# Optimization experiments

Hardware: AMD Instinct MI355X
Metric: run time of the kernel (lower is better)

The kernel has to match this reference:

```python
import jax, jax.numpy as jnp
import numpy as np

B, S, C = 4, 1024, 1024
HD = 64          # hard-coded head dim in the module
H = C // HD      # 16 heads
ROT = 32         # RotaryEmbedding hard-codes Dim=32 (partial rotary)
EPS = 1e-4       # pnormalize eps


def pnormalize(w, parts):
    # torch: reshape(parts, -1, *w.shape[1:]); vector_norm over trailing dims;
    # alpha = sqrt(n.numel()/partitioned.numel()) = 1/sqrt(fan_in); w / (eps + alpha*n)
    p = w.reshape(parts, -1, w.shape[-1])
    n = jnp.linalg.norm(p, axis=-1, keepdims=True)
    alpha = np.sqrt(n.size / p.size)
    return (p / (EPS + alpha * n)).reshape(w.shape)


def mp_linear(x, w, parts):
    fan_in = w.shape[-1]
    return x @ (pnormalize(w, parts) / np.sqrt(fan_in)).T


def rotate_half(t):
    t1, t2 = jnp.split(t, 2, axis=-1)
    return jnp.concatenate([-t2, t1], axis=-1)


def apply_rope(t, freqs):
    return t * jnp.cos(freqs) + rotate_half(t) * jnp.sin(freqs)


def setup_inputs() -> dict:
    key = jax.random.key(0)
    k1, k2, k3, k4 = jax.random.split(key, 4)
    x = jax.random.normal(k1, (B, S, C), jnp.float32)
    w_qkv = jax.random.normal(k2, (3 * C, C), jnp.float32)   # MPLinear init: std=1
    w_out = jax.random.normal(k3, (C, C), jnp.float32)
    sink = jax.random.normal(k4, (1, 1, C), jnp.float32)
    # rotary table: RotaryEmbedding with Dim=32
    inv_freq = 1.0 / (10000.0 ** (np.arange(0, ROT, 2, dtype=np.float32) / ROT))
    t = np.arange(S, dtype=np.float32)
    freqs = np.einsum('i,j->ij', t, inv_freq)          # (S, 16)
    re = jnp.asarray(np.concatenate([freqs, freqs], axis=-1)[None, None], jnp.float32)  # (1,1,S,32)
    # causal mask over S+1 tokens (sink appended last); sink row/col fully visible
    Sf = S + 1
    m = np.tril(np.ones((Sf, Sf), dtype=bool))
    m[:, -1] = True
    m[-1, :] = True
    attn_mask = jnp.asarray(m)
    return {"x": x, "re": re, "attn_mask": attn_mask, "w_qkv": w_qkv, "w_out": w_out, "sink": sink}


def reference(x, re, attn_mask, w_qkv, w_out, sink):
    Bn, Sn, Cn = x.shape
    Hn = Cn // HD
    # append sink token
    x = jnp.concatenate([x, jnp.broadcast_to(sink, (Bn, 1, Cn))], axis=1)  # (B, S+1, C)
    qkv = mp_linear(x, w_qkv, 3)
    q, k, v = jnp.split(qkv, 3, axis=-1)
    scale = HD ** (-0.25)
    heads = lambda t: t.reshape(Bn, -1, Hn, HD).transpose(0, 2, 1, 3)  # (B,H,S+1,64)
    q, k, v = heads(q * scale), heads(k * scale), heads(v)
    # partial rotary: only non-sink tokens, only first ROT dims of head
    q_s, k_s = q[:, :, -1:], k[:, :, -1:]
    qb, kb = q[:, :, :-1], k[:, :, :-1]
    l = re.shape[-1]
    qb = jnp.concatenate([apply_rope(qb[..., :l], re), qb[..., l:]], axis=-1)
    kb = jnp.concatenate([apply_rope(kb[..., :l], re), kb[..., l:]], axis=-1)
    q = jnp.concatenate([qb, q_s], axis=2)
    k = jnp.concatenate([kb, k_s], axis=2)
    # cosine attention: unit-normalize q, k over head dim
    q = q / jnp.linalg.norm(q, axis=-1, keepdims=True)
    k = k / jnp.linalg.norm(k, axis=-1, keepdims=True)
    M = jnp.einsum('bhid,bhjd->bhij', q, k)  # (B,H,S+1,S+1)
    Sf = q.shape[2]
    M = jnp.where(attn_mask[None, None, :Sf, :Sf], M, -jnp.inf)
    A = jax.nn.softmax(M, axis=-1)
    h = jnp.einsum('bhij,bhjd->bhid', A, v)
    h = h[:, :, :-1]  # drop sink output
    h = h.transpose(0, 2, 1, 3).reshape(Bn, Sn, Cn)
    # mag_norm (no-grad magnitude matching against post-sink input x)
    desired = jax.lax.stop_gradient(jnp.mean(jnp.linalg.norm(x, axis=-1)))
    current = jax.lax.stop_gradient(jnp.mean(jnp.linalg.norm(h, axis=-1)))
    h = h * (desired / current)
    return mp_linear(h, w_out, 1)
```

## Files before the change

kernel.cpp:

```cpp
#include <hip/hip_runtime.h>
#include <hip/hip_bf16.h>
#include <cstdint>

typedef __attribute__((ext_vector_type(8))) short short8;
typedef __attribute__((ext_vector_type(4))) float f32x4;

typedef const unsigned int __attribute__((address_space(1)))* gas_ptr;
typedef unsigned int __attribute__((address_space(3)))* las_ptr;

__device__ static inline void async16(const void* g, void* l) {
  __builtin_amdgcn_global_load_lds((gas_ptr)g, (las_ptr)l, 16, 0, 0);
}

__device__ static inline unsigned short f2bf(float f) {
  union { float f; uint32_t u; } v; v.f = f;
  uint32_t u = v.u;
  uint32_t r = (u + 0x7FFFu + ((u >> 16) & 1u)) >> 16;
  return (unsigned short)r;
}
__device__ static inline float bf2f(unsigned short s) {
  union { uint32_t u; float f; } v; v.u = ((uint32_t)s) << 16; return v.f;
}

__device__ static inline float wave_sum(float v) {
  v += __shfl_xor(v, 1);  v += __shfl_xor(v, 2);  v += __shfl_xor(v, 4);
  v += __shfl_xor(v, 8);  v += __shfl_xor(v, 16); v += __shfl_xor(v, 32);
  return v;
}

#define SBAR __builtin_amdgcn_sched_barrier(0)


__global__ __launch_bounds__(256) void k_init_trig(const float* __restrict__ re,
    float* __restrict__ ctT, float* __restrict__ stT, float* __restrict__ sc) {
  int i = blockIdx.x * 256 + threadIdx.x;
  if (i < 1040) sc[i] = 0.0f;
  int s = i >> 4, r = i & 15;
  float f = re[s * 32 + r];
  ctT[r * 1024 + s] = cosf(f);
  stT[r * 1024 + s] = sinf(f);
}

__global__ __launch_bounds__(256) void k_wnorm(const float* __restrict__ W,
                                               unsigned short* __restrict__ E, int rows) {
  int row = blockIdx.x * 4 + (threadIdx.x >> 6);
  int l = threadIdx.x & 63;
  if (row >= rows) return;
  const float* wr = W + (size_t)row * 1024;
  float4 v[4];
  float s = 0.f;
  for (int i = 0; i < 4; ++i) {
    v[i] = *(const float4*)(wr + i * 256 + l * 4);
    s += v[i].x * v[i].x + v[i].y * v[i].y + v[i].z * v[i].z + v[i].w * v[i].w;
  }
  s = wave_sum(s);
  float inv = 1.0f / (0.0032f + sqrtf(s));
  unsigned short* er = E + (size_t)row * 1024;
  for (int i = 0; i < 4; ++i) {
    ushort4 o = make_ushort4(f2bf(v[i].x * inv), f2bf(v[i].y * inv),
                             f2bf(v[i].z * inv), f2bf(v[i].w * inv));
    *(ushort4*)(er + i * 256 + l * 4) = o;
  }
}

__global__ __launch_bounds__(256) void k_xext(const float* __restrict__ x,
    const float* __restrict__ sink, unsigned short* __restrict__ Xe,
    float* __restrict__ sc) {
  __shared__ float red[4];
  const int row = blockIdx.x;
  const int tid = threadIdx.x, w = tid >> 6, l = tid & 63;
  const int c4 = tid * 4;
  float4 v = make_float4(0.f, 0.f, 0.f, 0.f);
  if (row < 4100) {
    int b = row / 1025, s = row - b * 1025;
    const float* src = (s < 1024) ? (x + ((size_t)(b * 1024 + s)) * 1024 + c4) : (sink + c4);
    v = *(const float4*)src;
  }
  *(ushort4*)(Xe + (size_t)row * 1024 + c4) =
      make_ushort4(f2bf(v.x), f2bf(v.y), f2bf(v.z), f2bf(v.w));
  float ss = v.x * v.x + v.y * v.y + v.z * v.z + v.w * v.w;
  ss = wave_sum(ss);
  if (l == 0) red[w] = ss;
  __syncthreads();
  if (tid == 0 && row < 4100)
    atomicAdd(sc + 16 + (row & 63) * 16, sqrtf(red[0] + red[1] + red[2] + red[3]));
}

__global__ __launch_bounds__(256) void k_rownormB(const unsigned short* __restrict__ Hb,
                                                  float* __restrict__ acc) {
  __shared__ float red[4];
  const int w = threadIdx.x >> 6, l = threadIdx.x & 63;
  float local = 0.f;
  for (int row = blockIdx.x * 4 + w; row < 4096; row += gridDim.x * 4) {
    const unsigned short* hr = Hb + (size_t)row * 1024;
    float s = 0.f;
    for (int i = 0; i < 2; ++i) {
      short8 v = *(const short8*)(hr + i * 512 + l * 8);
      #pragma unroll
      for (int k = 0; k < 8; ++k) { float f = bf2f((unsigned short)v[k]); s += f * f; }
    }
    s = wave_sum(s);
    local += sqrtf(s);
  }
  if (l == 0) red[w] = local;
  __syncthreads();
  if (threadIdx.x == 0)
    atomicAdd(acc, red[0] + red[1] + red[2] + red[3]);
}

template<int EPI>
__global__ __launch_bounds__(256, 4) void k_gemm128(
    const unsigned short* __restrict__ A, const unsigned short* __restrict__ B,
    float* __restrict__ C, int N, int K, int ntn,
    unsigned short* __restrict__ Qh, unsigned short* __restrict__ Kh,
    unsigned short* __restrict__ Vt,
    const float* __restrict__ ctT, const float* __restrict__ stT,
    const float* __restrict__ sc) {
  constexpr int BM = EPI ? 128 : 64;
  constexpr int MI = BM / 32;
  __shared__ __align__(16) short SMEM[(BM + 128) * 64];
  short* Al = SMEM;
  short* Bl = SMEM + BM * 64;
  const int t = threadIdx.x, l = t & 63, w = t >> 6;
  const int r = l & 15, g = l >> 4;
  const int wm = w >> 1, wn = w & 1;
  const int nwg = gridDim.x;
  const int q = nwg >> 3, rr = nwg & 7;
  const int xcd = blockIdx.x & 7, loc = blockIdx.x >> 3;
  const int wgid = (xcd < rr ? xcd * (q + 1) : rr * (q + 1) + (xcd - rr) * q) + loc;
  const int tm = wgid / ntn, tn = wgid % ntn;
  const size_t am0 = (size_t)tm * BM, bn0 = (size_t)tn * 128;

  f32x4 acc[MI][4] = {};
  for (int kt = 0; kt < K; kt += 64) {
    __syncthreads();
    #pragma unroll
    for (int i = 0; i < BM / 32; ++i) {
      int c = i * 256 + t;
      int row = c >> 3, sch = (c & 7) ^ (row & 7);
      async16(A + (am0 + row) * (size_t)K + kt + sch * 8, Al + (i * 256 + w * 64) * 8);
    }
    #pragma unroll
    for (int i = 0; i < 4; ++i) {
      int c = i * 256 + t;
      int row = c >> 3, sch = (c & 7) ^ (row & 7);
      async16(B + (bn0 + row) * (size_t)K + kt + sch * 8, Bl + (i * 256 + w * 64) * 8);
    }
    __syncthreads();
    #pragma unroll
    for (int ks = 0; ks < 2; ++ks) {
      short8 af[MI], bfr[4];
      #pragma unroll
      for (int mi = 0; mi < MI; ++mi) {
        const int arow = wm * (MI * 16) + mi * 16 + r;
        af[mi] = *(const short8*)(Al + arow * 64 + (((ks * 4 + g) ^ (arow & 7)) << 3));
      }
      #pragma unroll
      for (int ni = 0; ni < 4; ++ni) {
        const int brow = wn * 64 + ni * 16 + r;
        bfr[ni] = *(const short8*)(Bl + brow * 64 + (((ks * 4 + g) ^ (brow & 7)) << 3));
      }
      #pragma unroll
      for (int mi = 0; mi < MI; ++mi)
        #pragma unroll
        for (int ni = 0; ni < 4; ++ni)
          acc[mi][ni] = __builtin_amdgcn_mfma_f32_16x16x32_bf16(af[mi], bfr[ni], acc[mi][ni], 0, 0, 0);
    }
  }

  if constexpr (EPI == 0) {
    float num = 0.f;
    #pragma unroll
    for (int i = 0; i < 64; ++i) num += sc[16 + i * 16];
    const float ratio = (num * (1.0f / 4100.0f)) * (4096.0f / sc[1]);
    #pragma unroll
    for (int mi = 0; mi < MI; ++mi)
      #pragma unroll
      for (int ni = 0; ni < 4; ++ni)
        #pragma unroll
        for (int j = 0; j < 4; ++j) {
          size_t row = am0 + wm * (MI * 16) + mi * 16 + g * 4 + j;
          size_t col = bn0 + wn * 64 + ni * 16 + r;
          C[row * (size_t)N + col] = acc[mi][ni][j] * ratio;
        }
  } else {
    __syncthreads();
    const int head_global = tn * 2 + wn;
    const int sel = head_global >> 4;
    const int h = head_global & 15;
    const int row0 = (int)am0 + wm * 64;

    if (sel < 2) {
      unsigned short* dst = (sel == 0) ? Qh : Kh;
      #pragma unroll
      for (int mi = 0; mi < 4; ++mi) {
        const int rowb = row0 + mi * 16 + g * 4;
        const int b = rowb / 1025;
        const int s0 = rowb - b * 1025;
        float cs[4], sn[4];
        if (s0 + 3 < 1024) {
          float4 c4 = *(const float4*)(ctT + r * 1024 + s0);
          float4 s4 = *(const float4*)(stT + r * 1024 + s0);
          cs[0] = c4.x; cs[1] = c4.y; cs[2] = c4.z; cs[3] = c4.w;
          sn[0] = s4.x; sn[1] = s4.y; sn[2] = s4.z; sn[3] = s4.w;
        } else {
          #pragma unroll
          for (int j = 0; j < 4; ++j) {
            const int rj = rowb + j;
            const int bj = rj / 1025, sj = rj - bj * 1025;
            cs[j] = (sj < 1024) ? ctT[r * 1024 + sj] : 1.f;
            sn[j] = (sj < 1024) ? stT[r * 1024 + sj] : 0.f;
          }
        }
        #pragma unroll
        for (int j = 0; j < 4; ++j) {
          const int row = rowb + j;
          const int b2 = row / 1025, s = row - b2 * 1025;
          const float a0 = acc[mi][0][j], a1 = acc[mi][1][j];
          const float a2 = acc[mi][2][j], a3 = acc[mi][3][j];
          const float r0 = a0 * cs[j] - a1 * sn[j];
          const float r1 = a1 * cs[j] + a0 * sn[j];
          float nrm = r0 * r0 + r1 * r1 + a2 * a2 + a3 * a3;
          nrm += __shfl_xor(nrm, 1); nrm += __shfl_xor(nrm, 2);
          nrm += __shfl_xor(nrm, 4); nrm += __shfl_xor(nrm, 8);
          const float inv = rsqrtf(nrm);
          if (row < 4100) {
            const size_t base = ((size_t)(b2 * 16 + h) * 1088 + s) * 64 + r;
            dst[base]      = f2bf(r0 * inv);
            dst[base + 16] = f2bf(r1 * inv);
            dst[base + 32] = f2bf(a2 * inv);
            dst[base + 48] = f2bf(a3 * inv);
          }
        }
      }
    } else {
      short* vs = SMEM + w * 4096;
      #pragma unroll
      for (int mi = 0; mi < 4; ++mi) {
        const int slot = mi * 4 + g;
        #pragma unroll
        for (int ni = 0; ni < 4; ++ni) {
          const int d = ni * 16 + r;
          ushort4 pk = make_ushort4(f2bf(acc[mi][ni][0]), f2bf(acc[mi][ni][1]),
                                    f2bf(acc[mi][ni][2]), f2bf(acc[mi][ni][3]));
          *(ushort4*)(vs + d * 64 + ((slot ^ (d & 15)) << 2)) = pk;
        }
      }
      asm volatile("s_waitcnt lgkmcnt(0)" ::: "memory"); SBAR;
      #pragma unroll
      for (int ii = 0; ii < 16; ++ii) {
        const int d = ii * 4 + g;
        ushort4 vv = *(const ushort4*)(vs + d * 64 + (((r ^ (d & 15)) & 15) << 2));
        const int grow = row0 + r * 4;
        const int b0 = grow / 1025, b3 = (grow + 3) / 1025;
        if (b0 == b3 && grow + 3 < 4100) {
          const int s = grow - b0 * 1025;
          *(ushort4*)(Vt + ((size_t)(b0 * 16 + h) * 64 + d) * 1088 + s) = vv;
        } else {
          unsigned short tmp[4] = {vv.x, vv.y, vv.z, vv.w};
          for (int k2 = 0; k2 < 4; ++k2) {
            const int gr = grow + k2;
            if (gr >= 4100) break;
            const int bb = gr / 1025, ss = gr - bb * 1025;
            Vt[((size_t)(bb * 16 + h) * 64 + d) * 1088 + ss] = tmp[k2];
          }
        }
      }
    }
  }
}

__global__ __launch_bounds__(128) void k_attn(const unsigned short* __restrict__ Qh,
    const unsigned short* __restrict__ Kh, const unsigned short* __restrict__ Vt,
    unsigned short* __restrict__ Hb) {
  __shared__ __align__(16) short Kl[2][64 * 64];
  __shared__ __align__(16) short Vl[2][64 * 64];
  __shared__ __align__(16) short Pl[2 * 16 * 64];
  const int wid = blockIdx.x;
  const int xcd = wid & 7, jj = wid >> 3;
  const int bh = xcd + 8 * (jj >> 4), pp = jj & 15;
  const int b = bh >> 4, hh = bh & 15;
  const int t = threadIdx.x, l = t & 63, w = t >> 6;
  const int r = l & 15, g = l >> 4;

  auto stage = [&](int buf, int kt) {
    for (int i = 0; i < 4; ++i) {
      int c = i * 128 + t;
      int row = c >> 3, ch = c & 7;
      int sch = ch ^ (row & 7);
      async16(Kh + ((size_t)bh * 1088 + kt * 64 + row) * 64 + sch * 8,
              Kl[buf] + (i * 128 + w * 64) * 8);
      async16(Vt + ((size_t)bh * 64 + row) * 1088 + kt * 64 + sch * 8,
              Vl[buf] + (i * 128 + w * 64) * 8);
    }
  };

  for (int sidx = 0; sidx < 2; ++sidx) {
    const int strip = sidx == 0 ? pp : 31 - pp;
    const int qrow0 = strip * 32 + w * 16;
    short8 qf[2];
    for (int ks = 0; ks < 2; ++ks)
      qf[ks] = *(const short8*)(Qh + ((size_t)bh * 1088 + qrow0 + r) * 64 + ks * 32 + g * 8);
    const int nt = strip / 2 + 2;
    f32x4 oacc[4] = {};
    float lsum[4] = {0.f, 0.f, 0.f, 0.f};
    stage(0, 0);
    __syncthreads();
    int cur = 0;
    for (int i = 0; i < nt; ++i) {
      const int kt = (i < nt - 1) ? i : 16;
      if (i + 1 < nt) stage(cur ^ 1, (i + 1 < nt - 1) ? (i + 1) : 16);
      for (int nc = 0; nc < 4; ++nc) {
        f32x4 sc = {};
        for (int ks = 0; ks < 2; ++ks) {
          const int row = nc * 16 + r;
          const short8 kf = *(const short8*)(Kl[cur] + row * 64 + (((ks * 4 + g) ^ (row & 7)) << 3));
          sc = __builtin_amdgcn_mfma_f32_16x16x32_bf16(qf[ks], kf, sc, 0, 0, 0);
        }
        const int col = kt * 64 + nc * 16 + r;
        for (int j = 0; j < 4; ++j) {
          const int qrow = qrow0 + g * 4 + j;
          const bool valid = (col <= qrow) || (col == 1024);
          float p = valid ? __expf(sc[j]) : 0.0f;
          unsigned short pb = f2bf(p);
          lsum[j] += bf2f(pb);
          const int prow = w * 16 + g * 4 + j;
          const int bir = (nc * 16 + r) * 2;
          char* pd = (char*)Pl + prow * 128 + ((((unsigned)bir >> 4) ^ (prow & 7)) << 4) + (bir & 15);
          *(short*)pd = (short)pb;
        }
      }
      for (int ks = 0; ks < 2; ++ks) {
        const int prow = w * 16 + r;
        const short8 pf = *(const short8*)((char*)Pl + prow * 128 + (((ks * 4 + g) ^ (r & 7)) << 4));
        for (int nd = 0; nd < 4; ++nd) {
          const int vrow = nd * 16 + r;
          const short8 vf = *(const short8*)(Vl[cur] + vrow * 64 + (((ks * 4 + g) ^ (vrow & 7)) << 3));
          oacc[nd] = __builtin_amdgcn_mfma_f32_16x16x32_bf16(pf, vf, oacc[nd], 0, 0, 0);
        }
      }
      __syncthreads();
      cur ^= 1;
    }
    float inv[4];
    for (int j = 0; j < 4; ++j) {
      float v = lsum[j];
      v += __shfl_xor(v, 1); v += __shfl_xor(v, 2);
      v += __shfl_xor(v, 4); v += __shfl_xor(v, 8);
      inv[j] = 1.0f / v;
    }
    for (int nd = 0; nd < 4; ++nd)
      for (int j = 0; j < 4; ++j) {
        const int srow = qrow0 + g * 4 + j;
        Hb[((size_t)(b * 1024 + srow)) * 1024 + hh * 64 + nd * 16 + r] = f2bf(oacc[nd][j] * inv[j]);
      }
  }
}

extern "C" void kernel_launch(void* const* d_in, const int* in_sizes, int n_in,
                              void* d_out, int out_size, void* d_ws, size_t ws_size,
                              hipStream_t stream) {
  const float* x     = (const float*)d_in[0];
  const float* re    = (const float*)d_in[1];
  const float* w_qkv = (const float*)d_in[3];
  const float* w_out = (const float*)d_in[4];
  const float* sink  = (const float*)d_in[5];
  char* ws = (char*)d_ws;

  unsigned short* Wq  = (unsigned short*)(ws + 0);
  unsigned short* Wo  = (unsigned short*)(ws + 6291456);
  unsigned short* Xe  = (unsigned short*)(ws + 8388608);
  unsigned short* Hb  = (unsigned short*)(ws + 17301504);
  unsigned short* Qh  = (unsigned short*)(ws + 25690112);
  unsigned short* Kh  = (unsigned short*)(ws + 34603008);
  unsigned short* Vt  = (unsigned short*)(ws + 43515904);
  float*          ctT = (float*)(ws + 52428800);
  float*          stT = (float*)(ws + 52494336);
  float*          sc  = (float*)(ws + 52559872);
  float*          out = (float*)d_out;

  k_init_trig<<<64, 256, 0, stream>>>(re, ctT, stT, sc);
  k_wnorm<<<768, 256, 0, stream>>>(w_qkv, Wq, 3072);
  k_wnorm<<<256, 256, 0, stream>>>(w_out, Wo, 1024);
  k_xext<<<4352, 256, 0, stream>>>(x, sink, Xe, sc);
  k_gemm128<1><<<34 * 24, 256, 0, stream>>>(Xe, Wq, nullptr, 3072, 1024, 24,
                                            Qh, Kh, Vt, ctT, stT, sc);
  k_attn<<<1024, 128, 0, stream>>>(Qh, Kh, Vt, Hb);
  k_rownormB<<<256, 256, 0, stream>>>(Hb, sc + 1);
  k_gemm128<0><<<64 * 8, 256, 0, stream>>>(Hb, Wo, out, 1024, 1024, 8,
                                           nullptr, nullptr, nullptr, ctT, stT, sc);
}
```

Measured before the change: 119.6 us.

## Fuse prep kernels, run both attention strips concurrently, fold row norms into attention

Merges the trig-table, weight-normalize and x-extension kernels into one launch, and replaces atomic accumulation with per-row norm buffers. These are reduced by a small new kernel. The attention kernel now uses 256 threads so the two causal strips run in parallel waves within a block instead of one after the other. Waves with fewer key tiles sit idle through the shared loop and its barriers. The attention epilogue also writes per-head squared row norms of the fp32 output, which removes the separate pass that re-read Hb. This changes the norm numerics slightly, since it uses pre-bf16 values.

```diff
diff --git a/kernel.cpp b/kernel.cpp
--- a/kernel.cpp
+++ b/kernel.cpp
@@ -30,82 +30,82 @@
 
 #define SBAR __builtin_amdgcn_sched_barrier(0)
 
-
-__global__ __launch_bounds__(256) void k_init_trig(const float* __restrict__ re,
-    float* __restrict__ ctT, float* __restrict__ stT, float* __restrict__ sc) {
-  int i = blockIdx.x * 256 + threadIdx.x;
-  if (i < 1040) sc[i] = 0.0f;
-  int s = i >> 4, r = i & 15;
-  float f = re[s * 32 + r];
-  ctT[r * 1024 + s] = cosf(f);
-  stT[r * 1024 + s] = sinf(f);
-}
-
-__global__ __launch_bounds__(256) void k_wnorm(const float* __restrict__ W,
-                                               unsigned short* __restrict__ E, int rows) {
-  int row = blockIdx.x * 4 + (threadIdx.x >> 6);
-  int l = threadIdx.x & 63;
-  if (row >= rows) return;
-  const float* wr = W + (size_t)row * 1024;
-  float4 v[4];
-  float s = 0.f;
-  for (int i = 0; i < 4; ++i) {
-    v[i] = *(const float4*)(wr + i * 256 + l * 4);
-    s += v[i].x * v[i].x + v[i].y * v[i].y + v[i].z * v[i].z + v[i].w * v[i].w;
-  }
-  s = wave_sum(s);
-  float inv = 1.0f / (0.0032f + sqrtf(s));
-  unsigned short* er = E + (size_t)row * 1024;
-  for (int i = 0; i < 4; ++i) {
-    ushort4 o = make_ushort4(f2bf(v[i].x * inv), f2bf(v[i].y * inv),
-                             f2bf(v[i].z * inv), f2bf(v[i].w * inv));
-    *(ushort4*)(er + i * 256 + l * 4) = o;
-  }
-}
-
-__global__ __launch_bounds__(256) void k_xext(const float* __restrict__ x,
-    const float* __restrict__ sink, unsigned short* __restrict__ Xe,
-    float* __restrict__ sc) {
+__global__ __launch_bounds__(256) void k_prep(const float* __restrict__ x,
+    const float* __restrict__ sink, const float* __restrict__ re,
+    const float* __restrict__ w_qkv, const float* __restrict__ w_out,
+    unsigned short* __restrict__ Xe, unsigned short* __restrict__ Wq,
+    unsigned short* __restrict__ Wo,
+    float* __restrict__ ctT, float* __restrict__ stT, float* __restrict__ rowsn) {
   __shared__ float red[4];
-  const int row = blockIdx.x;
+  const int bid = blockIdx.x;
   const int tid = threadIdx.x, w = tid >> 6, l = tid & 63;
-  const int c4 = tid * 4;
-  float4 v = make_float4(0.f, 0.f, 0.f, 0.f);
-  if (row < 4100) {
-    int b = row / 1025, s = row - b * 1025;
-    const float* src = (s < 1024) ? (x + ((size_t)(b * 1024 + s)) * 1024 + c4) : (sink + c4);
-    v = *(const float4*)src;
-  }
-  *(ushort4*)(Xe + (size_t)row * 1024 + c4) =
-      make_ushort4(f2bf(v.x), f2bf(v.y), f2bf(v.z), f2bf(v.w));
-  float ss = v.x * v.x + v.y * v.y + v.z * v.z + v.w * v.w;
-  ss = wave_sum(ss);
-  if (l == 0) red[w] = ss;
+  if (bid < 4352) {
+    const int row = bid;
+    const int c4 = tid * 4;
+    float4 v = make_float4(0.f, 0.f, 0.f, 0.f);
+    if (row < 4100) {
+      int b = row / 1025, s = row - b * 1025;
+      const float* src = (s < 1024) ? (x + ((size_t)(b * 1024 + s)) * 1024 + c4) : (sink + c4);
+      v = *(const float4*)src;
+    }
+    *(ushort4*)(Xe + (size_t)row * 1024 + c4) =
+        make_ushort4(f2bf(v.x), f2bf(v.y), f2bf(v.z), f2bf(v.w));
+    float ss = v.x * v.x + v.y * v.y + v.z * v.z + v.w * v.w;
+    ss = wave_sum(ss);
+    if (l == 0) red[w] = ss;
+    __syncthreads();
+    if (tid == 0) rowsn[row] = (row < 4100) ? sqrtf(red[0] + red[1] + red[2] + red[3]) : 0.f;
+  } else if (bid < 4416) {
+    int i = (bid - 4352) * 256 + tid;
+    int s = i >> 4, r2 = i & 15;
+    float f = re[s * 32 + r2];
+    ctT[r2 * 1024 + s] = cosf(f);
+    stT[r2 * 1024 + s] = sinf(f);
+  } else {
+    const float* W; unsigned short* E; int row;
+    if (bid < 5184) { W = w_qkv; E = Wq; row = (bid - 4416) * 4 + w; }
+    else            { W = w_out; E = Wo; row = (bid - 5184) * 4 + w; }
+    const float* wr = W + (size_t)row * 1024;
+    float4 v[4];
+    float s = 0.f;
+    #pragma unroll
+    for (int i = 0; i < 4; ++i) {
+      v[i] = *(const float4*)(wr + i * 256 + l * 4);
+      s += v[i].x * v[i].x + v[i].y * v[i].y + v[i].z * v[i].z + v[i].w * v[i].w;
+    }
+    s = wave_sum(s);
+    float inv = 1.0f / (0.0032f + sqrtf(s));
+    unsigned short* er = E + (size_t)row * 1024;
+    #pragma unroll
+    for (int i = 0; i < 4; ++i) {
+      ushort4 o = make_ushort4(f2bf(v[i].x * inv), f2bf(v[i].y * inv),
+                               f2bf(v[i].z * inv), f2bf(v[i].w * inv));
+      *(ushort4*)(er + i * 256 + l * 4) = o;
+    }
+  }
+}
+
+__global__ __launch_bounds__(256) void k_rownormC(const float* __restrict__ rowsqp,
+    const float* __restrict__ rowsn, float* __restrict__ scp) {
+  __shared__ float red[4];
+  const int bid = blockIdx.x, t = threadIdx.x, w = t >> 6, l = t & 63;
+  const int row = bid * 256 + t;
+  const float4* rp = (const float4*)(rowsqp + (size_t)row * 16);
+  float4 a = rp[0], b = rp[1], c = rp[2], d = rp[3];
+  float s = a.x + a.y + a.z + a.w + b.x + b.y + b.z + b.w +
+            c.x + c.y + c.z + c.w + d.x + d.y + d.z + d.w;
+  float v = sqrtf(s);
+  v = wave_sum(v);
+  if (l == 0) red[w] = v;
   __syncthreads();
-  if (tid == 0 && row < 4100)
-    atomicAdd(sc + 16 + (row & 63) * 16, sqrtf(red[0] + red[1] + red[2] + red[3]));
-}
-
-__global__ __launch_bounds__(256) void k_rownormB(const unsigned short* __restrict__ Hb,
-                                                  float* __restrict__ acc) {
-  __shared__ float red[4];
-  const int w = threadIdx.x >> 6, l = threadIdx.x & 63;
-  float local = 0.f;
-  for (int row = blockIdx.x * 4 + w; row < 4096; row += gridDim.x * 4) {
-    const unsigned short* hr = Hb + (size_t)row * 1024;
-    float s = 0.f;
-    for (int i = 0; i < 2; ++i) {
-      short8 v = *(const short8*)(hr + i * 512 + l * 8);
-      #pragma unroll
-      for (int k = 0; k < 8; ++k) { float f = bf2f((unsigned short)v[k]); s += f * f; }
-    }
-    s = wave_sum(s);
-    local += sqrtf(s);
-  }
-  if (l == 0) red[w] = local;
+  if (t == 0) scp[16 + bid] = red[0] + red[1] + red[2] + red[3];
+  float u = 0.f;
+  for (int k = t; k < 272; k += 256) u += rowsn[bid * 272 + k];
+  u = wave_sum(u);
   __syncthreads();
-  if (threadIdx.x == 0)
-    atomicAdd(acc, red[0] + red[1] + red[2] + red[3]);
+  if (l == 0) red[w] = u;
+  __syncthreads();
+  if (t == 0) scp[bid] = red[0] + red[1] + red[2] + red[3];
 }
 
 template<int EPI>
@@ -115,7 +115,7 @@
     unsigned short* __restrict__ Qh, unsigned short* __restrict__ Kh,
     unsigned short* __restrict__ Vt,
     const float* __restrict__ ctT, const float* __restrict__ stT,
-    const float* __restrict__ sc) {
+    const float* __restrict__ scp) {
   constexpr int BM = EPI ? 128 : 64;
   constexpr int MI = BM / 32;
   __shared__ __align__(16) short SMEM[(BM + 128) * 64];
@@ -169,10 +169,10 @@
   }
 
   if constexpr (EPI == 0) {
-    float num = 0.f;
-    #pragma unroll
-    for (int i = 0; i < 64; ++i) num += sc[16 + i * 16];
-    const float ratio = (num * (1.0f / 4100.0f)) * (4096.0f / sc[1]);
+    float num = 0.f, den = 0.f;
+    #pragma unroll
+    for (int i = 0; i < 16; ++i) { num += scp[i]; den += scp[16 + i]; }
+    const float ratio = (num * (1.0f / 4100.0f)) * (4096.0f / den);
     #pragma unroll
     for (int mi = 0; mi < MI; ++mi)
       #pragma unroll
@@ -270,54 +270,59 @@
   }
 }
 
-__global__ __launch_bounds__(128) void k_attn(const unsigned short* __restrict__ Qh,
+__global__ __launch_bounds__(256) void k_attn(const unsigned short* __restrict__ Qh,
     const unsigned short* __restrict__ Kh, const unsigned short* __restrict__ Vt,
-    unsigned short* __restrict__ Hb) {
+    unsigned short* __restrict__ Hb, float* __restrict__ rowsqp) {
   __shared__ __align__(16) short Kl[2][64 * 64];
   __shared__ __align__(16) short Vl[2][64 * 64];
-  __shared__ __align__(16) short Pl[2 * 16 * 64];
+  __shared__ __align__(16) short Pl[64 * 64];
   const int wid = blockIdx.x;
   const int xcd = wid & 7, jj = wid >> 3;
   const int bh = xcd + 8 * (jj >> 4), pp = jj & 15;
   const int b = bh >> 4, hh = bh & 15;
   const int t = threadIdx.x, l = t & 63, w = t >> 6;
   const int r = l & 15, g = l >> 4;
+  const int strip = (w < 2) ? pp : 31 - pp;
+  const int qrow0 = strip * 32 + (w & 1) * 16;
+  const int myNc = strip / 2 + 1;
+  const int NTOT = (31 - pp) / 2 + 2;
 
   auto stage = [&](int buf, int kt) {
-    for (int i = 0; i < 4; ++i) {
-      int c = i * 128 + t;
-      int row = c >> 3, ch = c & 7;
-      int sch = ch ^ (row & 7);
+    #pragma unroll
+    for (int i = 0; i < 2; ++i) {
+      int c = i * 256 + t;
+      int row = c >> 3, sch = (c & 7) ^ (row & 7);
       async16(Kh + ((size_t)bh * 1088 + kt * 64 + row) * 64 + sch * 8,
-              Kl[buf] + (i * 128 + w * 64) * 8);
+              Kl[buf] + (i * 256 + w * 64) * 8);
       async16(Vt + ((size_t)bh * 64 + row) * 1088 + kt * 64 + sch * 8,
-              Vl[buf] + (i * 128 + w * 64) * 8);
+              Vl[buf] + (i * 256 + w * 64) * 8);
     }
   };
 
-  for (int sidx = 0; sidx < 2; ++sidx) {
-    const int strip = sidx == 0 ? pp : 31 - pp;
-    const int qrow0 = strip * 32 + w * 16;
-    short8 qf[2];
-    for (int ks = 0; ks < 2; ++ks)
-      qf[ks] = *(const short8*)(Qh + ((size_t)bh * 1088 + qrow0 + r) * 64 + ks * 32 + g * 8);
-    const int nt = strip / 2 + 2;
-    f32x4 oacc[4] = {};
-    float lsum[4] = {0.f, 0.f, 0.f, 0.f};
-    stage(0, 0);
-    __syncthreads();
-    int cur = 0;
-    for (int i = 0; i < nt; ++i) {
-      const int kt = (i < nt - 1) ? i : 16;
-      if (i + 1 < nt) stage(cur ^ 1, (i + 1 < nt - 1) ? (i + 1) : 16);
+  short8 qf[2];
+  #pragma unroll
+  for (int ks = 0; ks < 2; ++ks)
+    qf[ks] = *(const short8*)(Qh + ((size_t)bh * 1088 + qrow0 + r) * 64 + ks * 32 + g * 8);
+  f32x4 oacc[4] = {};
+  float lsum[4] = {0.f, 0.f, 0.f, 0.f};
+  stage(0, 0);
+  __syncthreads();
+  int cur = 0;
+  for (int i = 0; i < NTOT; ++i) {
+    const int kt = (i < NTOT - 1) ? i : 16;
+    if (i + 1 < NTOT) stage(cur ^ 1, (i + 1 < NTOT - 1) ? (i + 1) : 16);
+    const bool active = (i < myNc) || (i == NTOT - 1);
+    if (active) {
       for (int nc = 0; nc < 4; ++nc) {
         f32x4 sc = {};
+        #pragma unroll
         for (int ks = 0; ks < 2; ++ks) {
           const int row = nc * 16 + r;
           const short8 kf = *(const short8*)(Kl[cur] + row * 64 + (((ks * 4 + g) ^ (row & 7)) << 3));
           sc = __builtin_amdgcn_mfma_f32_16x16x32_bf16(qf[ks], kf, sc, 0, 0, 0);
         }
         const int col = kt * 64 + nc * 16 + r;
+        #pragma unroll
         for (int j = 0; j < 4; ++j) {
           const int qrow = qrow0 + g * 4 + j;
           const bool valid = (col <= qrow) || (col == 1024);
@@ -330,30 +335,42 @@
           *(short*)pd = (short)pb;
         }
       }
+      #pragma unroll
       for (int ks = 0; ks < 2; ++ks) {
         const int prow = w * 16 + r;
         const short8 pf = *(const short8*)((char*)Pl + prow * 128 + (((ks * 4 + g) ^ (r & 7)) << 4));
+        #pragma unroll
         for (int nd = 0; nd < 4; ++nd) {
           const int vrow = nd * 16 + r;
           const short8 vf = *(const short8*)(Vl[cur] + vrow * 64 + (((ks * 4 + g) ^ (vrow & 7)) << 3));
           oacc[nd] = __builtin_amdgcn_mfma_f32_16x16x32_bf16(pf, vf, oacc[nd], 0, 0, 0);
         }
       }
-      __syncthreads();
-      cur ^= 1;
-    }
-    float inv[4];
-    for (int j = 0; j < 4; ++j) {
-      float v = lsum[j];
-      v += __shfl_xor(v, 1); v += __shfl_xor(v, 2);
-      v += __shfl_xor(v, 4); v += __shfl_xor(v, 8);
-      inv[j] = 1.0f / v;
-    }
-    for (int nd = 0; nd < 4; ++nd)
-      for (int j = 0; j < 4; ++j) {
-        const int srow = qrow0 + g * 4 + j;
-        Hb[((size_t)(b * 1024 + srow)) * 1024 + hh * 64 + nd * 16 + r] = f2bf(oacc[nd][j] * inv[j]);
-      }
+    }
+    __syncthreads();
+    cur ^= 1;
+  }
+  float inv[4];
+  #pragma unroll
+  for (int j = 0; j < 4; ++j) {
+    float v = lsum[j];
+    v += __shfl_xor(v, 1); v += __shfl_xor(v, 2);
+    v += __shfl_xor(v, 4); v += __shfl_xor(v, 8);
+    inv[j] = 1.0f / v;
+  }
+  #pragma unroll
+  for (int j = 0; j < 4; ++j) {
+    const int srow = qrow0 + g * 4 + j;
+    float sq = 0.f;
+    #pragma unroll
+    for (int nd = 0; nd < 4; ++nd) {
+      const float hv = oacc[nd][j] * inv[j];
+      Hb[((size_t)(b * 1024 + srow)) * 1024 + hh * 64 + nd * 16 + r] = f2bf(hv);
+      sq += hv * hv;
+    }
+    sq += __shfl_xor(sq, 1); sq += __shfl_xor(sq, 2);
+    sq += __shfl_xor(sq, 4); sq += __shfl_xor(sq, 8);
+    if (r == 0) rowsqp[(size_t)(b * 1024 + srow) * 16 + hh] = sq;
   }
 }
 
@@ -367,26 +384,25 @@
   const float* sink  = (const float*)d_in[5];
   char* ws = (char*)d_ws;
 
-  unsigned short* Wq  = (unsigned short*)(ws + 0);
-  unsigned short* Wo  = (unsigned short*)(ws + 6291456);
-  unsigned short* Xe  = (unsigned short*)(ws + 8388608);
-  unsigned short* Hb  = (unsigned short*)(ws + 17301504);
-  unsigned short* Qh  = (unsigned short*)(ws + 25690112);
-  unsigned short* Kh  = (unsigned short*)(ws + 34603008);
-  unsigned short* Vt  = (unsigned short*)(ws + 43515904);
-  float*          ctT = (float*)(ws + 52428800);
-  float*          stT = (float*)(ws + 52494336);
-  float*          sc  = (float*)(ws + 52559872);
-  float*          out = (float*)d_out;
-
-  k_init_trig<<<64, 256, 0, stream>>>(re, ctT, stT, sc);
-  k_wnorm<<<768, 256, 0, stream>>>(w_qkv, Wq, 3072);
-  k_wnorm<<<256, 256, 0, stream>>>(w_out, Wo, 1024);
-  k_xext<<<4352, 256, 0, stream>>>(x, sink, Xe, sc);
+  unsigned short* Wq   = (unsigned short*)(ws + 0);
+  unsigned short* Wo   = (unsigned short*)(ws + 6291456);
+  unsigned short* Xe   = (unsigned short*)(ws + 8388608);
+  unsigned short* Hb   = (unsigned short*)(ws + 17301504);
+  unsigned short* Qh   = (unsigned short*)(ws + 25690112);
+  unsigned short* Kh   = (unsigned short*)(ws + 34603008);
+  unsigned short* Vt   = (unsigned short*)(ws + 43515904);
+  float*          ctT  = (float*)(ws + 52428800);
+  float*          stT  = (float*)(ws + 52494336);
+  float*          scp  = (float*)(ws + 52559872);
+  float*          rowsn  = (float*)(ws + 52560384);
+  float*          rowsqp = (float*)(ws + 52577792);
+  float*          out  = (float*)d_out;
+
+  k_prep<<<5440, 256, 0, stream>>>(x, sink, re, w_qkv, w_out, Xe, Wq, Wo, ctT, stT, rowsn);
   k_gemm128<1><<<34 * 24, 256, 0, stream>>>(Xe, Wq, nullptr, 3072, 1024, 24,
-                                            Qh, Kh, Vt, ctT, stT, sc);
-  k_attn<<<1024, 128, 0, stream>>>(Qh, Kh, Vt, Hb);
-  k_rownormB<<<256, 256, 0, stream>>>(Hb, sc + 1);
+                                            Qh, Kh, Vt, ctT, stT, scp);
+  k_attn<<<1024, 256, 0, stream>>>(Qh, Kh, Vt, Hb, rowsqp);
+  k_rownormC<<<16, 256, 0, stream>>>(rowsqp, rowsn, scp);
   k_gemm128<0><<<64 * 8, 256, 0, stream>>>(Hb, Wo, out, 1024, 1024, 8,
-                                           nullptr, nullptr, nullptr, ctT, stT, sc);
-}
+                                           nullptr, nullptr, nullptr, ctT, stT, scp);
+}
```

New measurement: 103.9 us. -13.1%, faster.
